# Optimization experiments

Measured on AMD Instinct MI355X. Metric: run time of the kernel, lower is better.

The kernel has to match this reference:

```python
import jax, jax.numpy as jnp
import numpy as np

N, E, G, D, FIN, L, ELAB = 150000, 600000, 8192, 128, 16, 4, 500000
BN_EPS = 1e-5


def _bn(h, g, b, rm, rv):
    # eval-mode BatchNorm1d with running stats
    return (h - rm) * g * jax.lax.rsqrt(rv + BN_EPS) + b


def _pool_max(h, batch):
    # global_max_pool; empty segments -> 0 (instead of -inf)
    p = jax.ops.segment_max(h, batch, num_segments=G)
    return jnp.where(jnp.isneginf(p), 0.0, p)


def setup_inputs() -> dict:
    key = jax.random.key(0)
    ks = jax.random.split(key, 24)
    s_in = 1.0 / np.sqrt(FIN)
    s_d = 1.0 / np.sqrt(D)
    inp = {
        "x": jax.random.normal(ks[0], (N, FIN), jnp.float32),
        "edge_index": jax.random.randint(ks[1], (2, E), 0, N, jnp.int32),
        "batch": jnp.sort(jax.random.randint(ks[2], (N,), 0, G, jnp.int32)),
        "edge_index_labeled": jax.random.randint(ks[3], (2, ELAB), 0, G, jnp.int32),
        "edge_label": jax.random.randint(ks[4], (ELAB,), 0, 2, jnp.int32),
        # initial node encoder + initial linear (num_classes == emb_sizes == D)
        "enc_W": jax.random.normal(ks[5], (FIN, D), jnp.float32) * s_in,
        "enc_b": jnp.zeros((D,), jnp.float32),
        "init_W": jax.random.normal(ks[6], (D, D), jnp.float32) * s_d,
        "init_b": jnp.zeros((D,), jnp.float32),
        # per-layer GIN params (stacked over L layers)
        "gin_eps": jnp.zeros((L,), jnp.float32),
        "W1": jax.random.normal(ks[7], (L, D, D), jnp.float32) * s_d,
        "b1": jnp.zeros((L, D), jnp.float32),
        "g1": jnp.ones((L, D), jnp.float32),
        "be1": jnp.zeros((L, D), jnp.float32),
        "rm1": jnp.zeros((L, D), jnp.float32),
        "rv1": jnp.ones((L, D), jnp.float32),
        "W2": jax.random.normal(ks[8], (L, D, D), jnp.float32) * s_d,
        "b2": jnp.zeros((L, D), jnp.float32),
        "g2": jnp.ones((L, D), jnp.float32),
        "be2": jnp.zeros((L, D), jnp.float32),
        "rm2": jnp.zeros((L, D), jnp.float32),
        "rv2": jnp.ones((L, D), jnp.float32),
        # per-layer linear applied to pooled features
        "lin_W": jax.random.normal(ks[9], (L, D, D), jnp.float32) * s_d,
        "lin_b": jnp.zeros((L, D), jnp.float32),
        # layer_post_mp: ReLU -> Linear(D,D) -> ReLU -> Linear(D,1)
        "post_W1": jax.random.normal(ks[10], (D, D), jnp.float32) * s_d,
        "post_b1": jnp.zeros((D,), jnp.float32),
        "post_W2": jax.random.normal(ks[11], (D, 1), jnp.float32) * s_d,
        "post_b2": jnp.zeros((1,), jnp.float32),
    }
    return inp


def reference(x, edge_index, batch, edge_index_labeled, edge_label,
              enc_W, enc_b, init_W, init_b, gin_eps,
              W1, b1, g1, be1, rm1, rv1,
              W2, b2, g2, be2, rm2, rv2,
              lin_W, lin_b, post_W1, post_b1, post_W2, post_b2):
    src, dst = edge_index[0], edge_index[1]

    # initial MLP (node encoder) -> [N, D]
    x_feat = x @ enc_W + enc_b

    # out = dropout(pool(initial_linear(x_feat)))  (dropout = identity, eval)
    out = _pool_max(x_feat @ init_W + init_b, batch)  # [G, D]

    for i in range(L):
        # GINConv: mlp((1 + eps) * x + sum_{j in N(i)} x_j)
        agg = jax.ops.segment_sum(x_feat[src], dst, num_segments=N)  # [N, D]
        h = (1.0 + gin_eps[i]) * x_feat + agg
        h = jax.nn.relu(_bn(h @ W1[i] + b1[i], g1[i], be1[i], rm1[i], rv1[i]))
        x_feat = jax.nn.relu(_bn(h @ W2[i] + b2[i], g2[i], be2[i], rm2[i], rv2[i]))
        # out += dropout(linear(pool(x_feat)))
        out = out + (_pool_max(x_feat, batch) @ lin_W[i] + lin_b[i])

    # layer_post_mp: ReLU -> Linear -> ReLU -> Linear(D,1)
    out = jax.nn.relu(out)
    out = jax.nn.relu(out @ post_W1 + post_b1)
    out = out @ post_W2 + post_b2  # [G, 1]

    # _apply_index gather + dot-product decode
    pred_pairs = out[edge_index_labeled]  # [2, ELAB, 1]
    pred = jnp.sum(pred_pairs[0] * pred_pairs[1], axis=-1)  # [ELAB]
    return pred, edge_label
```

## Files before the change

kernel.cpp:

```cpp
#include <hip/hip_runtime.h>

#define NN 150000
#define NP 150016
#define NE 600000
#define NG 8192
#define DD 128
#define FINN 16
#define NL 4
#define NEL 500000
#define BN_EPS 1e-5f
#define NB_SCAN 147

typedef __attribute__((ext_vector_type(8))) short bf16x8;
typedef __attribute__((ext_vector_type(4))) float f32x4;

__device__ inline short bfr(float x) {
    unsigned u = __builtin_bit_cast(unsigned, x);
    unsigned r = u + 0x7fffu + ((u >> 16) & 1u);
    return (short)(r >> 16);
}
__device__ inline float bf2f(short h) {
    return __builtin_bit_cast(float, ((unsigned)(unsigned short)h) << 16);
}

__global__ __launch_bounds__(256) void enc_kernel(const float* __restrict__ x,
                                                  const float* __restrict__ W,
                                                  const float* __restrict__ b,
                                                  float* __restrict__ out) {
    int t = threadIdx.x;
    int c4 = (t & 31) * 4;
    float4 wreg[16];
#pragma unroll
    for (int k = 0; k < 16; k++) wreg[k] = *(const float4*)&W[k * DD + c4];
    float4 bias = *(const float4*)&b[c4];
    int rbase = blockIdx.x * 128 + (t >> 5);
#pragma unroll
    for (int it = 0; it < 16; it++) {
        int row = rbase + it * 8;
        if (row >= NN) break;
        const float4* xr = (const float4*)(x + (size_t)row * FINN);
        float4 x0 = xr[0], x1 = xr[1], x2 = xr[2], x3 = xr[3];
        float xs[16] = {x0.x, x0.y, x0.z, x0.w, x1.x, x1.y, x1.z, x1.w,
                        x2.x, x2.y, x2.z, x2.w, x3.x, x3.y, x3.z, x3.w};
        float4 acc = bias;
#pragma unroll
        for (int k = 0; k < 16; k++) {
            acc.x += xs[k] * wreg[k].x;
            acc.y += xs[k] * wreg[k].y;
            acc.z += xs[k] * wreg[k].z;
            acc.w += xs[k] * wreg[k].w;
        }
        *(float4*)&out[(size_t)row * DD + c4] = acc;
    }
}

__global__ void prep_w_kernel(const float* __restrict__ initW, const float* __restrict__ W1,
                              const float* __restrict__ W2, bf16x8* __restrict__ Wph,
                              bf16x8* __restrict__ Wpl) {
    int tid = blockIdx.x * 256 + threadIdx.x;
    if (tid >= 9 * 2048) return;
    int mat = tid >> 11;
    int rem = tid & 2047;
    int kk = rem >> 9;
    int c = (rem >> 6) & 7;
    int lane = rem & 63;
    const float* Wm;
    if (mat == 0) Wm = initW;
    else if (mat <= 4) Wm = W1 + (size_t)(mat - 1) * DD * DD;
    else Wm = W2 + (size_t)(mat - 5) * DD * DD;
    int col = c * 16 + (lane & 15);
    int kbase = kk * 32 + (lane >> 4) * 8;
    bf16x8 oh, ol;
#pragma unroll
    for (int j = 0; j < 8; j++) {
        float v = Wm[(size_t)(kbase + j) * DD + col];
        short h = bfr(v);
        oh[j] = h;
        ol[j] = bfr(v - bf2f(h));
    }
    Wph[tid] = oh;
    Wpl[tid] = ol;
}

__global__ void prep_scb_kernel(const float* __restrict__ initb,
                                const float* __restrict__ b1, const float* __restrict__ g1,
                                const float* __restrict__ be1, const float* __restrict__ rm1,
                                const float* __restrict__ rv1,
                                const float* __restrict__ b2, const float* __restrict__ g2,
                                const float* __restrict__ be2, const float* __restrict__ rm2,
                                const float* __restrict__ rv2,
                                float* __restrict__ sc, float* __restrict__ bb) {
    int tid = blockIdx.x * 256 + threadIdx.x;
    if (tid >= 9 * DD) return;
    int mat = tid >> 7, d = tid & 127;
    float s, o;
    if (mat == 0) {
        s = 1.f;
        o = initb[d];
    } else {
        const float *b_, *g_, *be_, *rm_, *rv_;
        int i;
        if (mat <= 4) { i = mat - 1; b_ = b1; g_ = g1; be_ = be1; rm_ = rm1; rv_ = rv1; }
        else          { i = mat - 5; b_ = b2; g_ = g2; be_ = be2; rm_ = rm2; rv_ = rv2; }
        float t = g_[i * DD + d] * rsqrtf(rv_[i * DD + d] + BN_EPS);
        s = t;
        o = (b_[i * DD + d] - rm_[i * DD + d]) * t + be_[i * DD + d];
    }
    sc[tid] = s;
    bb[tid] = o;
}

__global__ void zero_int_kernel(int* __restrict__ p, int n) {
    int i = blockIdx.x * 256 + threadIdx.x;
    if (i < n) p[i] = 0;
}

__global__ void hist_kernel(const int* __restrict__ dst, int* __restrict__ deg) {
    int e = blockIdx.x * 256 + threadIdx.x;
    if (e < NE) atomicAdd(&deg[dst[e]], 1);
}

__global__ void scan_reduce_kernel(const int* __restrict__ deg, int* __restrict__ bsum) {
    __shared__ int s[256];
    int b = blockIdx.x, t = threadIdx.x;
    int base = b * 1024 + t * 4;
    int v = 0;
#pragma unroll
    for (int i = 0; i < 4; i++) {
        int idx = base + i;
        if (idx < NN) v += deg[idx];
    }
    s[t] = v;
    __syncthreads();
    for (int off = 128; off > 0; off >>= 1) {
        if (t < off) s[t] += s[t + off];
        __syncthreads();
    }
    if (t == 0) bsum[b] = s[0];
}

__global__ void scan_mid_kernel(const int* __restrict__ bsum, int* __restrict__ boff,
                                int* __restrict__ rowptrN) {
    __shared__ int s[256];
    int t = threadIdx.x;
    int v = (t < NB_SCAN) ? bsum[t] : 0;
    s[t] = v;
    __syncthreads();
    for (int off = 1; off < 256; off <<= 1) {
        int u = (t >= off) ? s[t - off] : 0;
        __syncthreads();
        s[t] += u;
        __syncthreads();
    }
    if (t < NB_SCAN) boff[t] = s[t] - v;
    if (t == 255) *rowptrN = s[255];
}

__global__ void scan_final_kernel(const int* __restrict__ deg, const int* __restrict__ boff,
                                  int* __restrict__ rowptr) {
    __shared__ int s[256];
    int b = blockIdx.x, t = threadIdx.x;
    int base = b * 1024 + t * 4;
    int v[4];
    int sum = 0;
#pragma unroll
    for (int i = 0; i < 4; i++) {
        int idx = base + i;
        v[i] = (idx < NN) ? deg[idx] : 0;
        sum += v[i];
    }
    s[t] = sum;
    __syncthreads();
    int my = sum;
    for (int off = 1; off < 256; off <<= 1) {
        int u = (t >= off) ? s[t - off] : 0;
        __syncthreads();
        s[t] += u;
        __syncthreads();
    }
    int excl = s[t] - my + boff[b];
#pragma unroll
    for (int i = 0; i < 4; i++) {
        int idx = base + i;
        if (idx < NN) rowptr[idx] = excl;
        excl += v[i];
    }
}

__global__ void copy_int_kernel(const int* __restrict__ a, int* __restrict__ b, int n) {
    int i = blockIdx.x * 256 + threadIdx.x;
    if (i < n) b[i] = a[i];
}

__global__ void fill_kernel(const int* __restrict__ src, const int* __restrict__ dst,
                            int* cursor, int* __restrict__ csr_src) {
    int e = blockIdx.x * 256 + threadIdx.x;
    if (e >= NE) return;
    int p = atomicAdd(&cursor[dst[e]], 1);
    csr_src[p] = src[e];
}

__global__ void gstart_kernel(const int* __restrict__ batch, int* __restrict__ gstart) {
    int n = blockIdx.x * 256 + threadIdx.x;
    if (n >= NN) return;
    int b = batch[n];
    int prev = (n == 0) ? -1 : batch[n - 1];
    for (int g = prev + 1; g <= b; g++) gstart[g] = n;
    if (n == NN - 1) {
        for (int g = b + 1; g <= NG; g++) gstart[g] = NN;
    }
}

__global__ __launch_bounds__(256) void agg_kernel(const f32x4* __restrict__ A4,
                                                  const int* __restrict__ rowptr,
                                                  const int* __restrict__ csr_src,
                                                  const float* __restrict__ gin_eps,
                                                  int li, f32x4* __restrict__ B4) {
    int n = blockIdx.x * 8 + (threadIdx.x >> 5);
    int c = threadIdx.x & 31;
    float e1 = 1.f + gin_eps[li];
    int s = rowptr[n], e = rowptr[n + 1];
    int base = n << 5;
    f32x4 acc = A4[base + c] * e1;
    int i = s;
    for (; i + 4 <= e; i += 4) {
        int j0 = csr_src[i];
        int j1 = csr_src[i + 1];
        int j2 = csr_src[i + 2];
        int j3 = csr_src[i + 3];
        f32x4 v0 = A4[(j0 << 5) + c];
        f32x4 v1 = A4[(j1 << 5) + c];
        f32x4 v2 = A4[(j2 << 5) + c];
        f32x4 v3 = A4[(j3 << 5) + c];
        acc += (v0 + v1) + (v2 + v3);
    }
    for (; i < e; i++) acc += A4[(csr_src[i] << 5) + c];
    B4[base + c] = acc;
}

template <int RELU>
__global__ __launch_bounds__(256) void mm_kernel(const float* __restrict__ A,
                                                 float* __restrict__ C,
                                                 const bf16x8* __restrict__ Wph,
                                                 const bf16x8* __restrict__ Wpl,
                                                 const float* __restrict__ sc,
                                                 const float* __restrict__ bb) {
    int lane = threadIdx.x & 63;
    int wid = threadIdx.x >> 6;
    int row0 = blockIdx.x * 128 + wid * 32;
    int r16 = lane & 15;
    int kg = lane >> 4;
    f32x4 acc[2][8];
#pragma unroll
    for (int m = 0; m < 2; m++)
#pragma unroll
        for (int c = 0; c < 8; c++) acc[m][c] = (f32x4){0.f, 0.f, 0.f, 0.f};
#pragma unroll
    for (int kk = 0; kk < 4; kk++) {
        bf16x8 ah[2], al[2];
#pragma unroll
        for (int m = 0; m < 2; m++) {
            const float* ap = A + (size_t)(row0 + m * 16 + r16) * DD + kk * 32 + kg * 8;
            float4 lo = *(const float4*)ap;
            float4 hi = *(const float4*)(ap + 4);
            float v[8] = {lo.x, lo.y, lo.z, lo.w, hi.x, hi.y, hi.z, hi.w};
            bf16x8 th, tl;
#pragma unroll
            for (int j = 0; j < 8; j++) {
                short h = bfr(v[j]);
                th[j] = h;
                tl[j] = bfr(v[j] - bf2f(h));
            }
            ah[m] = th;
            al[m] = tl;
        }
#pragma unroll
        for (int c = 0; c < 8; c++) {
            bf16x8 wh = Wph[kk * 512 + c * 64 + lane];
            bf16x8 wl = Wpl[kk * 512 + c * 64 + lane];
#pragma unroll
            for (int m = 0; m < 2; m++) {
                acc[m][c] = __builtin_amdgcn_mfma_f32_16x16x32_bf16(ah[m], wh, acc[m][c], 0, 0, 0);
                acc[m][c] = __builtin_amdgcn_mfma_f32_16x16x32_bf16(al[m], wh, acc[m][c], 0, 0, 0);
                acc[m][c] = __builtin_amdgcn_mfma_f32_16x16x32_bf16(ah[m], wl, acc[m][c], 0, 0, 0);
            }
        }
    }
#pragma unroll
    for (int c = 0; c < 8; c++) {
        int col = c * 16 + r16;
        float s = sc[col], o = bb[col];
#pragma unroll
        for (int m = 0; m < 2; m++) {
            int rbase = row0 + m * 16 + kg * 4;
#pragma unroll
            for (int j = 0; j < 4; j++) {
                int row = rbase + j;
                if (row < NN) {
                    float v = acc[m][c][j] * s + o;
                    if (RELU) v = fmaxf(v, 0.f);
                    C[(size_t)row * DD + col] = v;
                }
            }
        }
    }
}

__global__ __launch_bounds__(256) void mm2x_kernel(
    const float* __restrict__ Ain, float* __restrict__ Aout,
    const bf16x8* __restrict__ Wph1, const bf16x8* __restrict__ Wpl1,
    const bf16x8* __restrict__ Wph2, const bf16x8* __restrict__ Wpl2,
    const float* __restrict__ sc1, const float* __restrict__ bb1,
    const float* __restrict__ sc2, const float* __restrict__ bb2) {
    __shared__ float hl[128 * 128];
    int lane = threadIdx.x & 63;
    int wid = threadIdx.x >> 6;
    int row0 = blockIdx.x * 128 + wid * 32;
    int r16 = lane & 15;
    int kg = lane >> 4;
    f32x4 acc[2][8];
#pragma unroll
    for (int m = 0; m < 2; m++)
#pragma unroll
        for (int c = 0; c < 8; c++) acc[m][c] = (f32x4){0.f, 0.f, 0.f, 0.f};

#pragma unroll
    for (int kk = 0; kk < 4; kk++) {
        bf16x8 ah[2], al[2];
#pragma unroll
        for (int m = 0; m < 2; m++) {
            const float* ap = Ain + (size_t)(row0 + m * 16 + r16) * DD + kk * 32 + kg * 8;
            float4 lo = *(const float4*)ap;
            float4 hi = *(const float4*)(ap + 4);
            float v[8] = {lo.x, lo.y, lo.z, lo.w, hi.x, hi.y, hi.z, hi.w};
            bf16x8 th, tl;
#pragma unroll
            for (int j = 0; j < 8; j++) {
                short h = bfr(v[j]);
                th[j] = h;
                tl[j] = bfr(v[j] - bf2f(h));
            }
            ah[m] = th;
            al[m] = tl;
        }
#pragma unroll
        for (int c = 0; c < 8; c++) {
            bf16x8 wh = Wph1[kk * 512 + c * 64 + lane];
            bf16x8 wl = Wpl1[kk * 512 + c * 64 + lane];
#pragma unroll
            for (int m = 0; m < 2; m++) {
                acc[m][c] = __builtin_amdgcn_mfma_f32_16x16x32_bf16(ah[m], wh, acc[m][c], 0, 0, 0);
                acc[m][c] = __builtin_amdgcn_mfma_f32_16x16x32_bf16(al[m], wh, acc[m][c], 0, 0, 0);
                acc[m][c] = __builtin_amdgcn_mfma_f32_16x16x32_bf16(ah[m], wl, acc[m][c], 0, 0, 0);
            }
        }
    }
#pragma unroll
    for (int c = 0; c < 8; c++) {
        int col = c * 16 + r16;
        float s = sc1[col], o = bb1[col];
#pragma unroll
        for (int m = 0; m < 2; m++) {
#pragma unroll
            for (int j = 0; j < 4; j++) {
                int rl = wid * 32 + m * 16 + kg * 4 + j;
                float v = fmaxf(acc[m][c][j] * s + o, 0.f);
                hl[rl * 128 + (col ^ ((rl & 7) << 2))] = v;
            }
        }
    }
    __syncthreads();

#pragma unroll
    for (int m = 0; m < 2; m++)
#pragma unroll
        for (int c = 0; c < 8; c++) acc[m][c] = (f32x4){0.f, 0.f, 0.f, 0.f};
#pragma unroll
    for (int kk = 0; kk < 4; kk++) {
        bf16x8 ah[2], al[2];
#pragma unroll
        for (int m = 0; m < 2; m++) {
            int rl = wid * 32 + m * 16 + r16;
            int sw = (rl & 7) << 2;
            int c0 = kk * 32 + kg * 8;
            float4 lo = *(const float4*)&hl[rl * 128 + (c0 ^ sw)];
            float4 hi = *(const float4*)&hl[rl * 128 + ((c0 + 4) ^ sw)];
            float v[8] = {lo.x, lo.y, lo.z, lo.w, hi.x, hi.y, hi.z, hi.w};
            bf16x8 th, tl;
#pragma unroll
            for (int j = 0; j < 8; j++) {
                short h = bfr(v[j]);
                th[j] = h;
                tl[j] = bfr(v[j] - bf2f(h));
            }
            ah[m] = th;
            al[m] = tl;
        }
#pragma unroll
        for (int c = 0; c < 8; c++) {
            bf16x8 wh = Wph2[kk * 512 + c * 64 + lane];
            bf16x8 wl = Wpl2[kk * 512 + c * 64 + lane];
#pragma unroll
            for (int m = 0; m < 2; m++) {
                acc[m][c] = __builtin_amdgcn_mfma_f32_16x16x32_bf16(ah[m], wh, acc[m][c], 0, 0, 0);
                acc[m][c] = __builtin_amdgcn_mfma_f32_16x16x32_bf16(al[m], wh, acc[m][c], 0, 0, 0);
                acc[m][c] = __builtin_amdgcn_mfma_f32_16x16x32_bf16(ah[m], wl, acc[m][c], 0, 0, 0);
            }
        }
    }
#pragma unroll
    for (int c = 0; c < 8; c++) {
        int col = c * 16 + r16;
        float s = sc2[col], o = bb2[col];
#pragma unroll
        for (int m = 0; m < 2; m++) {
            int rbase = row0 + m * 16 + kg * 4;
#pragma unroll
            for (int j = 0; j < 4; j++) {
                int row = rbase + j;
                if (row < NN) {
                    Aout[(size_t)row * DD + col] = fmaxf(acc[m][c][j] * s + o, 0.f);
                }
            }
        }
    }
}

__global__ void pool0_kernel(const float* __restrict__ X, const int* __restrict__ gstart,
                             float* __restrict__ OUT) {
    int gph = blockIdx.x;
    int d = threadIdx.x;
    int start = gstart[gph], end = gstart[gph + 1];
    float m;
    if (start >= end) {
        m = 0.f;
    } else {
        m = -INFINITY;
        for (int n = start; n < end; n++) m = fmaxf(m, X[(size_t)n * DD + d]);
    }
    OUT[(size_t)gph * DD + d] = m;
}

__global__ __launch_bounds__(128) void poollin_kernel(const float* __restrict__ X,
                                                      const int* __restrict__ gstart,
                                                      const float* __restrict__ W,
                                                      const float* __restrict__ b,
                                                      float* __restrict__ OUT) {
    __shared__ float p[4][DD];
    int g0 = blockIdx.x * 4;
    int d = threadIdx.x;
#pragma unroll
    for (int gg = 0; gg < 4; gg++) {
        int start = gstart[g0 + gg], end = gstart[g0 + gg + 1];
        float m;
        if (start >= end) {
            m = 0.f;
        } else {
            m = -INFINITY;
            for (int n = start; n < end; n++) m = fmaxf(m, X[(size_t)n * DD + d]);
        }
        p[gg][d] = m;
    }
    __syncthreads();
    float acc0 = b[d], acc1 = b[d], acc2 = b[d], acc3 = b[d];
#pragma unroll 8
    for (int k = 0; k < DD; k++) {
        float w = W[k * DD + d];
        acc0 += p[0][k] * w;
        acc1 += p[1][k] * w;
        acc2 += p[2][k] * w;
        acc3 += p[3][k] * w;
    }
    OUT[(size_t)(g0 + 0) * DD + d] += acc0;
    OUT[(size_t)(g0 + 1) * DD + d] += acc1;
    OUT[(size_t)(g0 + 2) * DD + d] += acc2;
    OUT[(size_t)(g0 + 3) * DD + d] += acc3;
}

__global__ void post_kernel(const float* __restrict__ OUT, const float* __restrict__ W1,
                            const float* __restrict__ b1, const float* __restrict__ W2,
                            const float* __restrict__ b2, float* __restrict__ S) {
    __shared__ float o[DD];
    __shared__ float red[2];
    int gph = blockIdx.x, d = threadIdx.x;
    o[d] = fmaxf(OUT[(size_t)gph * DD + d], 0.f);
    __syncthreads();
    float acc = b1[d];
#pragma unroll 8
    for (int k = 0; k < DD; k++) acc += o[k] * W1[k * DD + d];
    acc = fmaxf(acc, 0.f);
    float v = acc * W2[d];
#pragma unroll
    for (int off = 32; off > 0; off >>= 1) v += __shfl_down(v, off);
    if ((d & 63) == 0) red[d >> 6] = v;
    __syncthreads();
    if (d == 0) S[gph] = red[0] + red[1] + b2[0];
}

__global__ void pred_kernel(const int* __restrict__ eil, const int* __restrict__ el,
                            const float* __restrict__ S, float* __restrict__ out) {
    int i = blockIdx.x * blockDim.x + threadIdx.x;
    if (i >= NEL) return;
    int a = eil[i], b = eil[NEL + i];
    out[i] = S[a] * S[b];
    out[NEL + i] = (float)el[i];
}

extern "C" void kernel_launch(void* const* d_in, const int* in_sizes, int n_in,
                              void* d_out, int out_size, void* d_ws, size_t ws_size,
                              hipStream_t stream) {
    const float* x = (const float*)d_in[0];
    const int* edge_index = (const int*)d_in[1];
    const int* batch = (const int*)d_in[2];
    const int* eil = (const int*)d_in[3];
    const int* el = (const int*)d_in[4];
    const float* encW = (const float*)d_in[5];
    const float* encb = (const float*)d_in[6];
    const float* initW = (const float*)d_in[7];
    const float* initb = (const float*)d_in[8];
    const float* gin_eps = (const float*)d_in[9];
    const float* W1 = (const float*)d_in[10];
    const float* b1 = (const float*)d_in[11];
    const float* g1 = (const float*)d_in[12];
    const float* be1 = (const float*)d_in[13];
    const float* rm1 = (const float*)d_in[14];
    const float* rv1 = (const float*)d_in[15];
    const float* W2 = (const float*)d_in[16];
    const float* b2 = (const float*)d_in[17];
    const float* g2 = (const float*)d_in[18];
    const float* be2 = (const float*)d_in[19];
    const float* rm2 = (const float*)d_in[20];
    const float* rv2 = (const float*)d_in[21];
    const float* linW = (const float*)d_in[22];
    const float* linb = (const float*)d_in[23];
    const float* postW1 = (const float*)d_in[24];
    const float* postb1 = (const float*)d_in[25];
    const float* postW2 = (const float*)d_in[26];
    const float* postb2 = (const float*)d_in[27];

    const int* srcArr = edge_index;
    const int* dstArr = edge_index + NE;

    char* w = (char*)d_ws;
    auto carve = [&](size_t bytes) -> char* {
        char* p = w;
        w += (bytes + 255) & ~(size_t)255;
        return p;
    };
    float* A = (float*)carve((size_t)NP * DD * 4);
    float* B = (float*)carve((size_t)NP * DD * 4);
    float* OUTb = (float*)carve((size_t)NG * DD * 4);
    float* S = (float*)carve((size_t)NG * 4);
    int* deg = (int*)carve((size_t)NN * 4);
    int* rowptr = (int*)carve((size_t)(NN + 1) * 4);
    int* cursor = (int*)carve((size_t)NN * 4);
    int* csr_src = (int*)carve((size_t)NE * 4);
    int* bsum = (int*)carve((size_t)NB_SCAN * 4);
    int* boff = (int*)carve((size_t)NB_SCAN * 4);
    int* gstart = (int*)carve((size_t)(NG + 1) * 4);
    bf16x8* Wph = (bf16x8*)carve((size_t)9 * 2048 * 16);
    bf16x8* Wpl = (bf16x8*)carve((size_t)9 * 2048 * 16);
    float* scv = (float*)carve((size_t)9 * DD * 4);
    float* bbv = (float*)carve((size_t)9 * DD * 4);

    float* out = (float*)d_out;
    const int mmBlk = NP / 128;

    prep_w_kernel<<<72, 256, 0, stream>>>(initW, W1, W2, Wph, Wpl);
    prep_scb_kernel<<<5, 256, 0, stream>>>(initb, b1, g1, be1, rm1, rv1,
                                           b2, g2, be2, rm2, rv2, scv, bbv);

    zero_int_kernel<<<586, 256, 0, stream>>>(deg, NN);
    hist_kernel<<<2344, 256, 0, stream>>>(dstArr, deg);
    scan_reduce_kernel<<<NB_SCAN, 256, 0, stream>>>(deg, bsum);
    scan_mid_kernel<<<1, 256, 0, stream>>>(bsum, boff, rowptr + NN);
    scan_final_kernel<<<NB_SCAN, 256, 0, stream>>>(deg, boff, rowptr);
    copy_int_kernel<<<586, 256, 0, stream>>>(rowptr, cursor, NN);
    fill_kernel<<<2344, 256, 0, stream>>>(srcArr, dstArr, cursor, csr_src);
    gstart_kernel<<<586, 256, 0, stream>>>(batch, gstart);

    enc_kernel<<<mmBlk, 256, 0, stream>>>(x, encW, encb, A);
    mm_kernel<0><<<mmBlk, 256, 0, stream>>>(A, B, Wph, Wpl, scv, bbv);
    pool0_kernel<<<NG, DD, 0, stream>>>(B, gstart, OUTb);

    for (int i = 0; i < NL; i++) {
        agg_kernel<<<NN / 8, 256, 0, stream>>>((const f32x4*)A, rowptr, csr_src,
                                               gin_eps, i, (f32x4*)B);
        mm2x_kernel<<<mmBlk, 256, 0, stream>>>(
            B, A,
            Wph + (size_t)(1 + i) * 2048, Wpl + (size_t)(1 + i) * 2048,
            Wph + (size_t)(5 + i) * 2048, Wpl + (size_t)(5 + i) * 2048,
            scv + (1 + i) * DD, bbv + (1 + i) * DD,
            scv + (5 + i) * DD, bbv + (5 + i) * DD);
        poollin_kernel<<<NG / 4, DD, 0, stream>>>(A, gstart, linW + (size_t)i * DD * DD,
                                                  linb + i * DD, OUTb);
    }

    post_kernel<<<NG, DD, 0, stream>>>(OUTb, postW1, postb1, postW2, postb2, S);
    pred_kernel<<<(NEL + 255) / 256, 256, 0, stream>>>(eil, el, S, out);
}
```

Baseline: 1.018 ms.

## Stage matmul input and output tiles through swizzled LDS for coalesced access

Both matmul kernels now load the 128x128 fp32 input tile into shared memory with fully coalesced 16-byte row loads, then build MFMA fragments from LDS. The output is first written to LDS and then stored to global memory as coalesced f32x4 rows, replacing the scattered per-element column stores. This targets the strided global loads and stores in these kernels, at the cost of extra barriers and LDS traffic. The input load is not bounds-checked and relies on the padded row count.

```diff
diff --git a/kernel.cpp b/kernel.cpp
--- a/kernel.cpp
+++ b/kernel.cpp
@@ -238,6 +238,22 @@
     B4[base + c] = acc;
 }
 
+
+__device__ inline void frag_from_lds(const f32x4* hl, int rl, int kk, int kg,
+                                     bf16x8& th, bf16x8& tl) {
+    int s = rl & 7;
+    int c0 = kk * 8 + kg * 2;
+    f32x4 lo = hl[rl * 32 + (c0 ^ s)];
+    f32x4 hi = hl[rl * 32 + ((c0 + 1) ^ s)];
+    float v[8] = {lo[0], lo[1], lo[2], lo[3], hi[0], hi[1], hi[2], hi[3]};
+#pragma unroll
+    for (int j = 0; j < 8; j++) {
+        short h = bfr(v[j]);
+        th[j] = h;
+        tl[j] = bfr(v[j] - bf2f(h));
+    }
+}
+
 template <int RELU>
 __global__ __launch_bounds__(256) void mm_kernel(const float* __restrict__ A,
                                                  float* __restrict__ C,
@@ -245,11 +261,21 @@
                                                  const bf16x8* __restrict__ Wpl,
                                                  const float* __restrict__ sc,
                                                  const float* __restrict__ bb) {
-    int lane = threadIdx.x & 63;
-    int wid = threadIdx.x >> 6;
-    int row0 = blockIdx.x * 128 + wid * 32;
-    int r16 = lane & 15;
-    int kg = lane >> 4;
+    __shared__ f32x4 hl[128 * 32];
+    float* hf = (float*)hl;
+    int t = threadIdx.x;
+    int lane = t & 63, wid = t >> 6;
+    int row0 = blockIdx.x * 128;
+    int r16 = lane & 15, kg = lane >> 4;
+    int sc4 = t & 31, srb = t >> 5;
+
+#pragma unroll
+    for (int it = 0; it < 16; it++) {
+        int r = it * 8 + srb;
+        hl[r * 32 + (sc4 ^ (r & 7))] = *(const f32x4*)&A[(size_t)(row0 + r) * DD + sc4 * 4];
+    }
+    __syncthreads();
+
     f32x4 acc[2][8];
 #pragma unroll
     for (int m = 0; m < 2; m++)
@@ -259,21 +285,8 @@
     for (int kk = 0; kk < 4; kk++) {
         bf16x8 ah[2], al[2];
 #pragma unroll
-        for (int m = 0; m < 2; m++) {
-            const float* ap = A + (size_t)(row0 + m * 16 + r16) * DD + kk * 32 + kg * 8;
-            float4 lo = *(const float4*)ap;
-            float4 hi = *(const float4*)(ap + 4);
-            float v[8] = {lo.x, lo.y, lo.z, lo.w, hi.x, hi.y, hi.z, hi.w};
-            bf16x8 th, tl;
-#pragma unroll
-            for (int j = 0; j < 8; j++) {
-                short h = bfr(v[j]);
-                th[j] = h;
-                tl[j] = bfr(v[j] - bf2f(h));
-            }
-            ah[m] = th;
-            al[m] = tl;
-        }
+        for (int m = 0; m < 2; m++)
+            frag_from_lds(hl, wid * 32 + m * 16 + r16, kk, kg, ah[m], al[m]);
 #pragma unroll
         for (int c = 0; c < 8; c++) {
             bf16x8 wh = Wph[kk * 512 + c * 64 + lane];
@@ -286,23 +299,29 @@
             }
         }
     }
+    __syncthreads();
 #pragma unroll
     for (int c = 0; c < 8; c++) {
         int col = c * 16 + r16;
         float s = sc[col], o = bb[col];
 #pragma unroll
         for (int m = 0; m < 2; m++) {
-            int rbase = row0 + m * 16 + kg * 4;
 #pragma unroll
             for (int j = 0; j < 4; j++) {
-                int row = rbase + j;
-                if (row < NN) {
-                    float v = acc[m][c][j] * s + o;
-                    if (RELU) v = fmaxf(v, 0.f);
-                    C[(size_t)row * DD + col] = v;
-                }
+                int rl = wid * 32 + m * 16 + kg * 4 + j;
+                float v = acc[m][c][j] * s + o;
+                if (RELU) v = fmaxf(v, 0.f);
+                hf[rl * 128 + (col ^ ((rl & 7) << 2))] = v;
             }
         }
+    }
+    __syncthreads();
+#pragma unroll
+    for (int it = 0; it < 16; it++) {
+        int r = it * 8 + srb;
+        int row = row0 + r;
+        if (row < NN)
+            *(f32x4*)&C[(size_t)row * DD + sc4 * 4] = hl[r * 32 + (sc4 ^ (r & 7))];
     }
 }
 
@@ -312,12 +331,21 @@
     const bf16x8* __restrict__ Wph2, const bf16x8* __restrict__ Wpl2,
     const float* __restrict__ sc1, const float* __restrict__ bb1,
     const float* __restrict__ sc2, const float* __restrict__ bb2) {
-    __shared__ float hl[128 * 128];
-    int lane = threadIdx.x & 63;
-    int wid = threadIdx.x >> 6;
-    int row0 = blockIdx.x * 128 + wid * 32;
-    int r16 = lane & 15;
-    int kg = lane >> 4;
+    __shared__ f32x4 hl[128 * 32];
+    float* hf = (float*)hl;
+    int t = threadIdx.x;
+    int lane = t & 63, wid = t >> 6;
+    int row0 = blockIdx.x * 128;
+    int r16 = lane & 15, kg = lane >> 4;
+    int sc4 = t & 31, srb = t >> 5;
+
+#pragma unroll
+    for (int it = 0; it < 16; it++) {
+        int r = it * 8 + srb;
+        hl[r * 32 + (sc4 ^ (r & 7))] = *(const f32x4*)&Ain[(size_t)(row0 + r) * DD + sc4 * 4];
+    }
+    __syncthreads();
+
     f32x4 acc[2][8];
 #pragma unroll
     for (int m = 0; m < 2; m++)
@@ -328,21 +356,8 @@
     for (int kk = 0; kk < 4; kk++) {
         bf16x8 ah[2], al[2];
 #pragma unroll
-        for (int m = 0; m < 2; m++) {
-            const float* ap = Ain + (size_t)(row0 + m * 16 + r16) * DD + kk * 32 + kg * 8;
-            float4 lo = *(const float4*)ap;
-            float4 hi = *(const float4*)(ap + 4);
-            float v[8] = {lo.x, lo.y, lo.z, lo.w, hi.x, hi.y, hi.z, hi.w};
-            bf16x8 th, tl;
-#pragma unroll
-            for (int j = 0; j < 8; j++) {
-                short h = bfr(v[j]);
-                th[j] = h;
-                tl[j] = bfr(v[j] - bf2f(h));
-            }
-            ah[m] = th;
-            al[m] = tl;
-        }
+        for (int m = 0; m < 2; m++)
+            frag_from_lds(hl, wid * 32 + m * 16 + r16, kk, kg, ah[m], al[m]);
 #pragma unroll
         for (int c = 0; c < 8; c++) {
             bf16x8 wh = Wph1[kk * 512 + c * 64 + lane];
@@ -355,6 +370,7 @@
             }
         }
     }
+    __syncthreads();
 #pragma unroll
     for (int c = 0; c < 8; c++) {
         int col = c * 16 + r16;
@@ -364,8 +380,7 @@
 #pragma unroll
             for (int j = 0; j < 4; j++) {
                 int rl = wid * 32 + m * 16 + kg * 4 + j;
-                float v = fmaxf(acc[m][c][j] * s + o, 0.f);
-                hl[rl * 128 + (col ^ ((rl & 7) << 2))] = v;
+                hf[rl * 128 + (col ^ ((rl & 7) << 2))] = fmaxf(acc[m][c][j] * s + o, 0.f);
             }
         }
     }
@@ -379,23 +394,8 @@
     for (int kk = 0; kk < 4; kk++) {
         bf16x8 ah[2], al[2];
 #pragma unroll
-        for (int m = 0; m < 2; m++) {
-            int rl = wid * 32 + m * 16 + r16;
-            int sw = (rl & 7) << 2;
-            int c0 = kk * 32 + kg * 8;
-            float4 lo = *(const float4*)&hl[rl * 128 + (c0 ^ sw)];
-            float4 hi = *(const float4*)&hl[rl * 128 + ((c0 + 4) ^ sw)];
-            float v[8] = {lo.x, lo.y, lo.z, lo.w, hi.x, hi.y, hi.z, hi.w};
-            bf16x8 th, tl;
-#pragma unroll
-            for (int j = 0; j < 8; j++) {
-                short h = bfr(v[j]);
-                th[j] = h;
-                tl[j] = bfr(v[j] - bf2f(h));
-            }
-            ah[m] = th;
-            al[m] = tl;
-        }
+        for (int m = 0; m < 2; m++)
+            frag_from_lds(hl, wid * 32 + m * 16 + r16, kk, kg, ah[m], al[m]);
 #pragma unroll
         for (int c = 0; c < 8; c++) {
             bf16x8 wh = Wph2[kk * 512 + c * 64 + lane];
@@ -408,21 +408,27 @@
             }
         }
     }
+    __syncthreads();
 #pragma unroll
     for (int c = 0; c < 8; c++) {
         int col = c * 16 + r16;
         float s = sc2[col], o = bb2[col];
 #pragma unroll
         for (int m = 0; m < 2; m++) {
-            int rbase = row0 + m * 16 + kg * 4;
 #pragma unroll
             for (int j = 0; j < 4; j++) {
-                int row = rbase + j;
-                if (row < NN) {
-                    Aout[(size_t)row * DD + col] = fmaxf(acc[m][c][j] * s + o, 0.f);
-                }
+                int rl = wid * 32 + m * 16 + kg * 4 + j;
+                hf[rl * 128 + (col ^ ((rl & 7) << 2))] = fmaxf(acc[m][c][j] * s + o, 0.f);
             }
         }
+    }
+    __syncthreads();
+#pragma unroll
+    for (int it = 0; it < 16; it++) {
+        int r = it * 8 + srb;
+        int row = row0 + r;
+        if (row < NN)
+            *(f32x4*)&Aout[(size_t)row * DD + sc4 * 4] = hl[r * 32 + (sc4 ^ (r & 7))];
     }
 }
 
```

New measurement: 1.129 ms. 1.11x slower.
